# Kernel optimization log

Hardware: AMD Instinct MI355X
Metric: run time of the kernel (lower is better)

The kernel has to match this reference:

```python
import jax, jax.numpy as jnp
import numpy as np

B, L, D, H, FF, V, NL = 1024, 200, 128, 4, 512, 100001, 2
DK = D // H
EPS = 1e-5


def layer_norm(x, w, b):
    mu = jnp.mean(x, axis=-1, keepdims=True)
    var = jnp.mean(jnp.square(x - mu), axis=-1, keepdims=True)
    return (x - mu) * jax.lax.rsqrt(var + EPS) * w + b


def setup_inputs() -> dict:
    key = jax.random.key(0)
    ks = jax.random.split(key, 32)
    s = 0.02
    d = {}
    d["batch_seqs"] = jax.random.randint(ks[0], (B, L), 0, V, dtype=jnp.int32)
    d["token_emb"] = jax.random.normal(ks[1], (V, D), jnp.float32) * s
    d["pos_emb"] = jax.random.normal(ks[2], (L, D), jnp.float32) * s
    # per-layer stacked params, leading axis = layer
    d["Wq"] = jax.random.normal(ks[3], (NL, D, D), jnp.float32) * s
    d["bq"] = jnp.zeros((NL, D), jnp.float32)
    d["Wk"] = jax.random.normal(ks[4], (NL, D, D), jnp.float32) * s
    d["bk"] = jnp.zeros((NL, D), jnp.float32)
    d["Wv"] = jax.random.normal(ks[5], (NL, D, D), jnp.float32) * s
    d["bv"] = jnp.zeros((NL, D), jnp.float32)
    d["Wo"] = jax.random.normal(ks[6], (NL, D, D), jnp.float32) * s
    d["bo"] = jnp.zeros((NL, D), jnp.float32)
    d["ln1_w"] = jnp.ones((NL, D), jnp.float32)
    d["ln1_b"] = jnp.zeros((NL, D), jnp.float32)
    d["ln2_w"] = jnp.ones((NL, D), jnp.float32)
    d["ln2_b"] = jnp.zeros((NL, D), jnp.float32)
    d["W1"] = jax.random.normal(ks[7], (NL, D, FF), jnp.float32) * s
    d["b1"] = jnp.zeros((NL, FF), jnp.float32)
    d["W2"] = jax.random.normal(ks[8], (NL, FF, D), jnp.float32) * s
    d["b2"] = jnp.zeros((NL, D), jnp.float32)
    d["fc_W"] = jax.random.normal(ks[9], (L * D, D), jnp.float32) * s
    d["fc_b"] = jnp.zeros((D,), jnp.float32)
    return d


def reference(batch_seqs, token_emb, pos_emb, Wq, bq, Wk, bk, Wv, bv, Wo, bo,
              ln1_w, ln1_b, ln2_w, ln2_b, W1, b1, W2, b2, fc_W, fc_b):
    # key-padding mask: [B,1,1,L] (broadcasts over heads and queries)
    mask = (batch_seqs > 0)[:, None, None, :]
    x = token_emb[batch_seqs] + pos_emb[None, :, :]  # [B,L,D]
    scale = 1.0 / jnp.sqrt(jnp.float32(DK))
    for i in range(NL):
        h = layer_norm(x, ln1_w[i], ln1_b[i])
        q = (h @ Wq[i] + bq[i]).reshape(B, L, H, DK)
        k = (h @ Wk[i] + bk[i]).reshape(B, L, H, DK)
        v = (h @ Wv[i] + bv[i]).reshape(B, L, H, DK)
        scores = jnp.einsum('bqhd,bkhd->bhqk', q, k) * scale
        scores = jnp.where(mask, scores, -1e9)
        p = jax.nn.softmax(scores, axis=-1)
        attn = jnp.einsum('bhqk,bkhd->bqhd', p, v).reshape(B, L, D)
        x = x + (attn @ Wo[i] + bo[i])
        h = layer_norm(x, ln2_w[i], ln2_b[i])
        ffn = jax.nn.gelu(h @ W1[i] + b1[i], approximate=False) @ W2[i] + b2[i]
        x = x + ffn
    # FlattenLayers: flatten [B, L*D] -> Linear -> [B, D]
    out = x.reshape(B, L * D) @ fc_W + fc_b
    return out
```

## Files before the change

kernel.cpp:

```cpp
#include <hip/hip_runtime.h>
#include <math.h>

typedef unsigned short u16;
typedef unsigned int u32;
typedef __attribute__((ext_vector_type(8))) short bf16x8;
typedef __attribute__((ext_vector_type(4))) float f32x4;

#define Bx 1024
#define Lx 200
#define Dx 128
#define FFx 512
#define Mx (Bx*Lx)
#define PVP 232
#define TSP 40

__device__ __forceinline__ u16 f2bf(float f) {
  u32 u = __float_as_uint(f);
  u32 r = (u + 0x7fffu + ((u >> 16) & 1u)) >> 16;
  return (u16)r;
}

__device__ __forceinline__ float gelu_f(float v) {
  float z = v * fmaf(v * v, 0.0713548163f, 1.5957691216f);
  float e = __expf(-z);
  return v * __builtin_amdgcn_rcpf(1.0f + e);
}

union BFCV { u32 u[4]; bf16x8 h; };

struct CvtJobs {
  const float* src[13];
  u16* dst[13];
  int N[13];
  int ks[13];
  int bstart[14];
};

__global__ void k_cvt_all(CvtJobs J) {
  const int b = blockIdx.x;
  int j = 0;
  #pragma unroll 1
  while (b >= J.bstart[j + 1]) ++j;
  const float* __restrict__ src = J.src[j];
  u16* __restrict__ dst = J.dst[j];
  const int N = J.N[j], k_steps = J.ks[j];
  int id = (b - J.bstart[j]) * 256 + threadIdx.x;
  int lane = id & 63;
  int rest = id >> 6;
  int kst = rest % k_steps;
  int ntile = rest / k_steps;
  int n = ntile * 16 + (lane & 15);
  int kb = kst * 32 + ((lane >> 4) << 3);
  const float* sp = src + (size_t)kb * N + n;
  u32 w[4];
  #pragma unroll
  for (int jj = 0; jj < 4; ++jj) {
    u32 lo = f2bf(sp[(size_t)(2 * jj) * N]);
    u32 hi = f2bf(sp[(size_t)(2 * jj + 1) * N]);
    w[jj] = lo | (hi << 16);
  }
  ((uint4*)dst)[id] = make_uint4(w[0], w[1], w[2], w[3]);
}

__global__ void k_embed(const int* __restrict__ seq, const float* __restrict__ tok,
                        const float* __restrict__ pos, float* __restrict__ x) {
  const int i = blockIdx.x * 256 + threadIdx.x;
  const int row = i >> 5, c = i & 31;
  const int t = seq[row];
  const int l = row % Lx;
  const float4 a = ((const float4*)tok)[(size_t)t * 32 + c];
  const float4 p = ((const float4*)pos)[l * 32 + c];
  ((float4*)x)[i] = make_float4(a.x + p.x, a.y + p.y, a.z + p.z, a.w + p.w);
}

__device__ __forceinline__ void reg_ln(const float* __restrict__ xr,
                                       const float* __restrict__ ln_w,
                                       const float* __restrict__ ln_b,
                                       int quad, bf16x8 af[4]) {
  float v[32];
  float s = 0.f, sq = 0.f;
  #pragma unroll
  for (int kst = 0; kst < 4; ++kst) {
    float4 a = *(const float4*)(xr + kst * 32);
    float4 b = *(const float4*)(xr + kst * 32 + 4);
    v[kst * 8 + 0] = a.x; v[kst * 8 + 1] = a.y; v[kst * 8 + 2] = a.z; v[kst * 8 + 3] = a.w;
    v[kst * 8 + 4] = b.x; v[kst * 8 + 5] = b.y; v[kst * 8 + 6] = b.z; v[kst * 8 + 7] = b.w;
  }
  #pragma unroll
  for (int i = 0; i < 32; ++i) { s += v[i]; sq = fmaf(v[i], v[i], sq); }
  s  += __shfl_xor(s, 16);  s  += __shfl_xor(s, 32);
  sq += __shfl_xor(sq, 16); sq += __shfl_xor(sq, 32);
  float mu = s * 0.0078125f;
  float rr = rsqrtf(fmaf(-mu, mu, sq * 0.0078125f) + 1e-5f);
  #pragma unroll
  for (int kst = 0; kst < 4; ++kst) {
    const float* lwp = ln_w + kst * 32 + quad * 8;
    const float* lbp = ln_b + kst * 32 + quad * 8;
    float4 lw0 = *(const float4*)(lwp);
    float4 lw1 = *(const float4*)(lwp + 4);
    float4 lb0 = *(const float4*)(lbp);
    float4 lb1 = *(const float4*)(lbp + 4);
    float hw[8] = {lw0.x, lw0.y, lw0.z, lw0.w, lw1.x, lw1.y, lw1.z, lw1.w};
    float hb[8] = {lb0.x, lb0.y, lb0.z, lb0.w, lb1.x, lb1.y, lb1.z, lb1.w};
    BFCV cv;
    #pragma unroll
    for (int j = 0; j < 4; ++j) {
      float h0 = fmaf((v[kst * 8 + 2 * j]     - mu) * rr, hw[2 * j],     hb[2 * j]);
      float h1 = fmaf((v[kst * 8 + 2 * j + 1] - mu) * rr, hw[2 * j + 1], hb[2 * j + 1]);
      cv.u[j] = (u32)f2bf(h0) | ((u32)f2bf(h1) << 16);
    }
    af[kst] = cv.h;
  }
}

__global__ __launch_bounds__(256, 4)
void k_qkv(const float* __restrict__ x, const float* __restrict__ ln_w,
           const float* __restrict__ ln_b, const u16* __restrict__ Wqkvs,
           const float* __restrict__ bq, const float* __restrict__ bk,
           const float* __restrict__ bv,
           u16* __restrict__ qo, u16* __restrict__ ko, u16* __restrict__ vo) {
  const int tid = threadIdx.x;
  const int row0 = blockIdx.x * 64;
  const int lane = tid & 63, wv = tid >> 6;
  const int l15 = lane & 15, quad = lane >> 4;
  const int m0 = wv * 16;

  bf16x8 af[4];
  reg_ln(x + (size_t)(row0 + m0 + l15) * Dx + quad * 8, ln_w, ln_b, quad, af);

  int bl[4], ll[4];
  #pragma unroll
  for (int r = 0; r < 4; ++r) {
    int gr = row0 + m0 + quad * 4 + r;
    bl[r] = gr / 200;
    ll[r] = gr - bl[r] * 200;
  }

  const float scale = 0.17677669529663687f;
  #pragma unroll
  for (int nt = 0; nt < 24; ++nt) {
    f32x4 acc = (f32x4){0.f, 0.f, 0.f, 0.f};
    const u16* wb = Wqkvs + ((size_t)(nt * 4) * 64 + lane) * 8;
    #pragma unroll
    for (int kst = 0; kst < 4; ++kst) {
      bf16x8 bfr = *(const bf16x8*)(wb + kst * 64 * 8);
      acc = __builtin_amdgcn_mfma_f32_16x16x32_bf16(af[kst], bfr, acc, 0, 0, 0);
    }
    const int col = (nt & 7) * 16 + l15;
    const int head = col >> 5, dk = col & 31;
    if (nt < 8) {
      float bb = bq[col];
      #pragma unroll
      for (int r = 0; r < 4; ++r)
        qo[((size_t)(bl[r] * 4 + head) * 200 + ll[r]) * 32 + dk] = f2bf((acc[r] + bb) * scale);
    } else if (nt < 16) {
      float bb = bk[col];
      #pragma unroll
      for (int r = 0; r < 4; ++r)
        ko[((size_t)(bl[r] * 4 + head) * 200 + ll[r]) * 32 + dk] = f2bf(acc[r] + bb);
    } else {
      float bb = bv[col];
      #pragma unroll
      for (int r = 0; r < 4; ++r)
        vo[((size_t)(bl[r] * 4 + head) * 200 + ll[r]) * 32 + dk] = f2bf(acc[r] + bb);
    }
  }
}

__global__ __launch_bounds__(256, 3)
void k_attn2(const u16* __restrict__ q, const u16* __restrict__ k,
             const u16* __restrict__ v, const int* __restrict__ seq,
             u16* __restrict__ attn) {
  __shared__ float smask[224];
  __shared__ __align__(16) u16 vt[32 * PVP];
  __shared__ __align__(16) u16 Pb[4][16 * PVP];
  const int tid = threadIdx.x;
  const int bl = blockIdx.x >> 3, head = (blockIdx.x >> 1) & 3;
  const int bh = blockIdx.x >> 1;
  const int half = blockIdx.x & 1;
  const int lane = tid & 63, wv = tid >> 6;
  const int l15 = lane & 15, quad = lane >> 4;

  if (tid < 224)
    smask[tid] = (tid < 200 && seq[bl * 200 + tid] > 0) ? 0.f : -1e9f;
  #pragma unroll 1
  for (int e = tid; e < 800; e += 256) {
    int l = e >> 2, g = (e & 3) * 8;
    uint4 pv = *(const uint4*)(v + ((size_t)bh * 200 + l) * 32 + g);
    const u16* pw = (const u16*)&pv;
    #pragma unroll
    for (int j = 0; j < 8; ++j) vt[(g + j) * PVP + l] = pw[j];
  }
  #pragma unroll 1
  for (int e = tid; e < 1024; e += 256) {
    int rr = e >> 5, cc = 200 + (e & 31);
    vt[rr * PVP + cc] = 0;
  }
  __syncthreads();

  float msk[14];
  #pragma unroll
  for (int nt = 0; nt < 14; ++nt) msk[nt] = smask[nt * 16 + l15];

  const u16* qbase = q + (size_t)bh * 200 * 32;
  const u16* kbase = k + (size_t)bh * 200 * 32;
  u16* Pw = Pb[wv];

  const int mt0 = half ? 7 : 0;
  const int mte = half ? 13 : 7;
  #pragma unroll 1
  for (int mt = mt0 + wv; mt < mte; mt += 4) {
    bf16x8 qf = *(const bf16x8*)(qbase + (mt * 16 + l15) * 32 + quad * 8);
    f32x4 s[14];
    #pragma unroll
    for (int nt = 0; nt < 14; ++nt) {
      bf16x8 kf = *(const bf16x8*)(kbase + (nt * 16 + l15) * 32 + quad * 8);
      s[nt] = __builtin_amdgcn_mfma_f32_16x16x32_bf16(qf, kf, (f32x4){0.f, 0.f, 0.f, 0.f}, 0, 0, 0);
    }
    float rmax[4] = {-1e30f, -1e30f, -1e30f, -1e30f};
    #pragma unroll
    for (int nt = 0; nt < 14; ++nt) {
      #pragma unroll
      for (int r = 0; r < 4; ++r) {
        s[nt][r] += msk[nt];
        rmax[r] = fmaxf(rmax[r], s[nt][r]);
      }
    }
    #pragma unroll
    for (int m = 1; m < 16; m <<= 1) {
      #pragma unroll
      for (int r = 0; r < 4; ++r) rmax[r] = fmaxf(rmax[r], __shfl_xor(rmax[r], m));
    }
    float rsum[4] = {0.f, 0.f, 0.f, 0.f};
    #pragma unroll
    for (int nt = 0; nt < 14; ++nt) {
      #pragma unroll
      for (int r = 0; r < 4; ++r) {
        float p = __expf(s[nt][r] - rmax[r]);
        s[nt][r] = p;
        rsum[r] += p;
      }
    }
    #pragma unroll
    for (int m = 1; m < 16; m <<= 1) {
      #pragma unroll
      for (int r = 0; r < 4; ++r) rsum[r] += __shfl_xor(rsum[r], m);
    }
    float inv[4];
    #pragma unroll
    for (int r = 0; r < 4; ++r) inv[r] = 1.0f / rsum[r];
    #pragma unroll
    for (int nt = 0; nt < 14; ++nt) {
      #pragma unroll
      for (int r = 0; r < 4; ++r)
        Pw[(quad * 4 + r) * PVP + nt * 16 + l15] = f2bf(s[nt][r]);
    }
    __asm__ __volatile__("s_waitcnt lgkmcnt(0)" ::: "memory");
    f32x4 o0 = (f32x4){0.f, 0.f, 0.f, 0.f}, o1 = (f32x4){0.f, 0.f, 0.f, 0.f};
    #pragma unroll
    for (int kst = 0; kst < 7; ++kst) {
      bf16x8 pf  = *(const bf16x8*)&Pw[l15 * PVP + kst * 32 + quad * 8];
      bf16x8 vf0 = *(const bf16x8*)&vt[l15 * PVP + kst * 32 + quad * 8];
      bf16x8 vf1 = *(const bf16x8*)&vt[(16 + l15) * PVP + kst * 32 + quad * 8];
      o0 = __builtin_amdgcn_mfma_f32_16x16x32_bf16(pf, vf0, o0, 0, 0, 0);
      o1 = __builtin_amdgcn_mfma_f32_16x16x32_bf16(pf, vf1, o1, 0, 0, 0);
    }
    #pragma unroll
    for (int r = 0; r < 4; ++r) {
      int row = mt * 16 + quad * 4 + r;
      if (row < 200) {
        u16* op = attn + ((size_t)bl * 200 + row) * 128 + head * 32;
        op[l15]      = f2bf(o0[r] * inv[r]);
        op[16 + l15] = f2bf(o1[r] * inv[r]);
      }
    }
  }
}

__global__ __launch_bounds__(256, 4)
void k_oproj(const u16* __restrict__ a, const u16* __restrict__ Wos,
             const float* __restrict__ bo, float* __restrict__ x) {
  const int tid = threadIdx.x;
  const int lane = tid & 63, wv = tid >> 6;
  const int l15 = lane & 15, quad = lane >> 4;
  const size_t m0 = (size_t)blockIdx.x * 64 + wv * 16;
  f32x4 acc[8];
  #pragma unroll
  for (int i = 0; i < 8; ++i) acc[i] = (f32x4){0.f, 0.f, 0.f, 0.f};
  #pragma unroll
  for (int kst = 0; kst < 4; ++kst) {
    bf16x8 af = *(const bf16x8*)(a + (m0 + l15) * Dx + kst * 32 + quad * 8);
    const u16* wb = Wos + (kst * 64 + lane) * 8;
    #pragma unroll
    for (int nt = 0; nt < 8; ++nt) {
      bf16x8 bf = *(const bf16x8*)(wb + nt * (4 * 64 * 8));
      acc[nt] = __builtin_amdgcn_mfma_f32_16x16x32_bf16(af, bf, acc[nt], 0, 0, 0);
    }
  }
  #pragma unroll
  for (int nt = 0; nt < 8; ++nt) {
    int col = nt * 16 + l15;
    float bb = bo[col];
    #pragma unroll
    for (int r = 0; r < 4; ++r) {
      size_t idx = (m0 + quad * 4 + r) * Dx + col;
      x[idx] += acc[nt][r] + bb;
    }
  }
}

__global__ __launch_bounds__(512, 4)
void k_ffn(float* __restrict__ x, const float* __restrict__ ln_w,
           const float* __restrict__ ln_b,
           const u16* __restrict__ W1s, const float* __restrict__ b1,
           const u16* __restrict__ W2s, const float* __restrict__ b2) {
  __shared__ __align__(16) u16 smem[5120 + 8192 + 8192];
  u16* ts  = smem;
  u16* w1b = smem + 5120;
  u16* w2b = smem + 13312;
  const int tid = threadIdx.x;
  const size_t row0 = (size_t)blockIdx.x * 128;
  const int lane = tid & 63, wv = tid >> 6;
  const int l15 = lane & 15, quad = lane >> 4;
  const int m0 = wv * 16;
  const int snt = wv, soff = lane;

  bf16x8 af[4];
  reg_ln(x + (row0 + m0 + l15) * (size_t)Dx + quad * 8, ln_w, ln_b, quad, af);

  ((uint4*)w1b)[tid] = ((const uint4*)(W1s + (size_t)(snt * 4) * 512))[soff];
  ((uint4*)w2b)[tid] = ((const uint4*)(W2s + (size_t)(snt * 16) * 512))[soff];
  __syncthreads();

  f32x4 acc2[8];
  #pragma unroll
  for (int i = 0; i < 8; ++i) acc2[i] = (f32x4){0.f, 0.f, 0.f, 0.f};

  #pragma unroll 1
  for (int ch = 0; ch < 4; ++ch) {
    f32x4 acc1[8];
    #pragma unroll
    for (int i = 0; i < 8; ++i) acc1[i] = (f32x4){0.f, 0.f, 0.f, 0.f};
    #pragma unroll
    for (int kst = 0; kst < 4; ++kst) {
      uint4 stg;
      if (kst < 3)
        stg = ((const uint4*)(W1s + (size_t)((ch * 8 + snt) * 4 + kst + 1) * 512))[soff];
      const u16* wb = w1b + (kst & 1) * 4096;
      #pragma unroll
      for (int nt = 0; nt < 8; ++nt) {
        bf16x8 bfr = *(const bf16x8*)&wb[nt * 512 + lane * 8];
        acc1[nt] = __builtin_amdgcn_mfma_f32_16x16x32_bf16(af[kst], bfr, acc1[nt], 0, 0, 0);
      }
      if (kst < 3)
        ((uint4*)(w1b + ((kst + 1) & 1) * 4096))[tid] = stg;
      __syncthreads();
    }
    #pragma unroll
    for (int p = 0; p < 4; ++p) {
      uint4 stg2, stg1;
      const bool s2  = (p < 3);
      const bool s1n = (p == 3) && (ch < 3);
      if (s2)
        stg2 = ((const uint4*)(W2s + (size_t)(snt * 16 + ch * 4 + p + 1) * 512))[soff];
      if (s1n) {
        stg1 = ((const uint4*)(W1s + (size_t)((ch + 1) * 8 + snt) * 4 * 512))[soff];
        stg2 = ((const uint4*)(W2s + (size_t)(snt * 16 + (ch + 1) * 4) * 512))[soff];
      }
      #pragma unroll
      for (int q2 = 0; q2 < 2; ++q2) {
        const int ntg = 2 * p + q2;
        float bb = b1[ch * 128 + ntg * 16 + l15];
        #pragma unroll
        for (int r = 0; r < 4; ++r)
          ts[(m0 + quad * 4 + r) * TSP + q2 * 16 + l15] =
              f2bf(gelu_f(acc1[ntg][r] + bb));
      }
      __asm__ __volatile__("s_waitcnt lgkmcnt(0)" ::: "memory");
      bf16x8 tf = *(const bf16x8*)&ts[(m0 + l15) * TSP + quad * 8];
      const u16* wb = w2b + (p & 1) * 4096;
      #pragma unroll
      for (int nt = 0; nt < 8; ++nt) {
        bf16x8 bfr = *(const bf16x8*)&wb[nt * 512 + lane * 8];
        acc2[nt] = __builtin_amdgcn_mfma_f32_16x16x32_bf16(tf, bfr, acc2[nt], 0, 0, 0);
      }
      if (s2)
        ((uint4*)(w2b + ((p + 1) & 1) * 4096))[tid] = stg2;
      if (s1n) {
        ((uint4*)w1b)[tid] = stg1;
        ((uint4*)w2b)[tid] = stg2;
      }
      __syncthreads();
    }
  }
  #pragma unroll
  for (int nt = 0; nt < 8; ++nt) {
    int col = nt * 16 + l15;
    float bb = b2[col];
    #pragma unroll
    for (int r = 0; r < 4; ++r) {
      size_t idx = (row0 + m0 + quad * 4 + r) * Dx + col;
      x[idx] += acc2[nt][r] + bb;
    }
  }
}

__global__ __launch_bounds__(256, 4)
void k_fc(const float* __restrict__ x, const u16* __restrict__ fcWs,
          float* __restrict__ part) {
  const int tid = threadIdx.x;
  const int lane = tid & 63, wv = tid >> 6;
  const int l15 = lane & 15, quad = lane >> 4;
  const int m0 = blockIdx.x * 64 + wv * 16;
  const int ky = blockIdx.y;
  f32x4 acc[8];
  #pragma unroll
  for (int i = 0; i < 8; ++i) acc[i] = (f32x4){0.f, 0.f, 0.f, 0.f};
  const float* xp = x + (size_t)(m0 + l15) * 25600 + quad * 8;
  #pragma unroll 1
  for (int kst = ky * 25; kst < ky * 25 + 25; ++kst) {
    float4 xa = *(const float4*)(xp + kst * 32);
    float4 xb2 = *(const float4*)(xp + kst * 32 + 4);
    bf16x8 af;
    af[0] = (short)f2bf(xa.x);  af[1] = (short)f2bf(xa.y);
    af[2] = (short)f2bf(xa.z);  af[3] = (short)f2bf(xa.w);
    af[4] = (short)f2bf(xb2.x); af[5] = (short)f2bf(xb2.y);
    af[6] = (short)f2bf(xb2.z); af[7] = (short)f2bf(xb2.w);
    const u16* wb = fcWs + ((size_t)kst * 64 + lane) * 8;
    #pragma unroll
    for (int nt = 0; nt < 8; ++nt) {
      bf16x8 bf = *(const bf16x8*)(wb + (size_t)nt * (800 * 64 * 8));
      acc[nt] = __builtin_amdgcn_mfma_f32_16x16x32_bf16(af, bf, acc[nt], 0, 0, 0);
    }
  }
  float* pp = part + (size_t)ky * (Bx * Dx);
  #pragma unroll
  for (int nt = 0; nt < 8; ++nt) {
    #pragma unroll
    for (int r = 0; r < 4; ++r) {
      pp[(size_t)(m0 + quad * 4 + r) * Dx + nt * 16 + l15] = acc[nt][r];
    }
  }
}

__global__ void k_fcred(const float* __restrict__ part, const float* __restrict__ fcb,
                        float* __restrict__ out) {
  int i = blockIdx.x * 256 + threadIdx.x;
  float s = fcb[i & 127];
  #pragma unroll
  for (int k = 0; k < 32; ++k) s += part[(size_t)k * (Bx * Dx) + i];
  out[i] = s;
}

extern "C" void kernel_launch(void* const* d_in, const int* in_sizes, int n_in,
                              void* d_out, int out_size, void* d_ws, size_t ws_size,
                              hipStream_t stream) {
  const int*   seq  = (const int*)d_in[0];
  const float* tok  = (const float*)d_in[1];
  const float* pos  = (const float*)d_in[2];
  const float* Wq   = (const float*)d_in[3];
  const float* bq   = (const float*)d_in[4];
  const float* Wk   = (const float*)d_in[5];
  const float* bk   = (const float*)d_in[6];
  const float* Wv   = (const float*)d_in[7];
  const float* bv   = (const float*)d_in[8];
  const float* Wo   = (const float*)d_in[9];
  const float* bo   = (const float*)d_in[10];
  const float* ln1w = (const float*)d_in[11];
  const float* ln1b = (const float*)d_in[12];
  const float* ln2w = (const float*)d_in[13];
  const float* ln2b = (const float*)d_in[14];
  const float* W1   = (const float*)d_in[15];
  const float* b1   = (const float*)d_in[16];
  const float* W2   = (const float*)d_in[17];
  const float* b2   = (const float*)d_in[18];
  const float* fcW  = (const float*)d_in[19];
  const float* fcb  = (const float*)d_in[20];
  float* out = (float*)d_out;

  char* ws = (char*)d_ws;
  const size_t XB = (size_t)Mx * Dx * 4;
  const size_t WBSZ = 7340032;

  int nc = 4;
  for (int t = 1; t <= 4; t <<= 1) {
    size_t qsz = (size_t)(Bx / t) * 51200;
    if (XB + 4 * qsz + WBSZ <= ws_size) { nc = t; break; }
  }
  const int BC = Bx / nc;
  const size_t qsz = (size_t)BC * 51200;

  float* x    = (float*)ws;
  u16* qb     = (u16*)(ws + XB);
  u16* kb     = (u16*)(ws + XB + qsz);
  u16* vb     = (u16*)(ws + XB + 2 * qsz);
  u16* ab     = (u16*)(ws + XB + 3 * qsz);
  float* part = (float*)(ws + XB);
  char* WB    = ws + XB + 4 * qsz;
  u16* W1s0   = (u16*)(WB);
  u16* W1s1   = (u16*)(WB + 131072);
  u16* W2s0   = (u16*)(WB + 262144);
  u16* W2s1   = (u16*)(WB + 393216);
  u16* Wos0   = (u16*)(WB + 524288);
  u16* Wos1   = (u16*)(WB + 557056);
  u16* Wqkvs0 = (u16*)(WB + 589824);
  u16* Wqkvs1 = (u16*)(WB + 688128);
  u16* fcWs   = (u16*)(WB + 786432);

  CvtJobs J;
  const float* srcs[13] = {W1, W1 + Dx * FFx, W2, W2 + FFx * Dx,
                           Wo, Wo + Dx * Dx,
                           Wq, Wk, Wv,
                           Wq + Dx * Dx, Wk + Dx * Dx, Wv + Dx * Dx,
                           fcW};
  u16* dsts[13] = {W1s0, W1s1, W2s0, W2s1, Wos0, Wos1,
                   Wqkvs0, Wqkvs0 + 16384, Wqkvs0 + 32768,
                   Wqkvs1, Wqkvs1 + 16384, Wqkvs1 + 32768,
                   fcWs};
  const int Ns[13]  = {FFx, FFx, Dx, Dx, Dx, Dx, Dx, Dx, Dx, Dx, Dx, Dx, Dx};
  const int kss[13] = {4, 4, 16, 16, 4, 4, 4, 4, 4, 4, 4, 4, 800};
  const int nblk[13] = {32, 32, 32, 32, 8, 8, 8, 8, 8, 8, 8, 8, 1600};
  int acc = 0;
  for (int j = 0; j < 13; ++j) {
    J.src[j] = srcs[j]; J.dst[j] = dsts[j]; J.N[j] = Ns[j]; J.ks[j] = kss[j];
    J.bstart[j] = acc; acc += nblk[j];
  }
  J.bstart[13] = acc;
  k_cvt_all<<<acc, 256, 0, stream>>>(J);

  k_embed<<<25600, 256, 0, stream>>>(seq, tok, pos, x);
  const int cblk = BC * 200 / 64;
  for (int i = 0; i < 2; ++i) {
    const u16* Wqkvs = (i == 0) ? Wqkvs0 : Wqkvs1;
    const u16* Wos   = (i == 0) ? Wos0 : Wos1;
    for (int c = 0; c < nc; ++c) {
      float* xc = x + (size_t)c * BC * 200 * 128;
      const int* seqc = seq + (size_t)c * BC * 200;
      k_qkv<<<cblk, 256, 0, stream>>>(xc, ln1w + i * Dx, ln1b + i * Dx, Wqkvs,
                                      bq + i * Dx, bk + i * Dx, bv + i * Dx,
                                      qb, kb, vb);
      k_attn2<<<BC * 8, 256, 0, stream>>>(qb, kb, vb, seqc, ab);
      k_oproj<<<cblk, 256, 0, stream>>>(ab, Wos, bo + i * Dx, xc);
    }
    k_ffn<<<1600, 512, 0, stream>>>(x, ln2w + i * Dx, ln2b + i * Dx,
                                    (i == 0) ? W1s0 : W1s1, b1 + i * FFx,
                                    (i == 0) ? W2s0 : W2s1, b2 + i * Dx);
  }
  k_fc<<<dim3(16, 32), 256, 0, stream>>>(x, fcWs, part);
  k_fcred<<<512, 256, 0, stream>>>(part, fcb, out);
}
```

Before: 988.9 us.

## Merge attention query halves per block and halve FFN block size

The attention kernel now handles all 13 query tiles of one (batch, head) in a single block instead of splitting them across two blocks. This avoids loading and transposing V and building the mask twice per head, at the cost of half as many blocks. The FFN kernel moves from 512-thread blocks over 128 rows to 256-thread blocks over 64 rows. Each thread now stages two weight vectors per step, which shrinks the transpose scratch buffer and doubles the grid, but each block reloads the full weights for fewer rows.

```diff
diff --git a/kernel.cpp b/kernel.cpp
--- a/kernel.cpp
+++ b/kernel.cpp
@@ -175,9 +175,8 @@
   __shared__ __align__(16) u16 vt[32 * PVP];
   __shared__ __align__(16) u16 Pb[4][16 * PVP];
   const int tid = threadIdx.x;
-  const int bl = blockIdx.x >> 3, head = (blockIdx.x >> 1) & 3;
-  const int bh = blockIdx.x >> 1;
-  const int half = blockIdx.x & 1;
+  const int bl = blockIdx.x >> 2, head = blockIdx.x & 3;
+  const int bh = blockIdx.x;
   const int lane = tid & 63, wv = tid >> 6;
   const int l15 = lane & 15, quad = lane >> 4;
 
@@ -206,10 +205,8 @@
   const u16* kbase = k + (size_t)bh * 200 * 32;
   u16* Pw = Pb[wv];
 
-  const int mt0 = half ? 7 : 0;
-  const int mte = half ? 13 : 7;
   #pragma unroll 1
-  for (int mt = mt0 + wv; mt < mte; mt += 4) {
+  for (int mt = wv; mt < 13; mt += 4) {
     bf16x8 qf = *(const bf16x8*)(qbase + (mt * 16 + l15) * 32 + quad * 8);
     f32x4 s[14];
     #pragma unroll
@@ -309,27 +306,29 @@
   }
 }
 
-__global__ __launch_bounds__(512, 4)
+__global__ __launch_bounds__(256, 4)
 void k_ffn(float* __restrict__ x, const float* __restrict__ ln_w,
            const float* __restrict__ ln_b,
            const u16* __restrict__ W1s, const float* __restrict__ b1,
            const u16* __restrict__ W2s, const float* __restrict__ b2) {
-  __shared__ __align__(16) u16 smem[5120 + 8192 + 8192];
+  __shared__ __align__(16) u16 smem[2560 + 8192 + 8192];
   u16* ts  = smem;
-  u16* w1b = smem + 5120;
-  u16* w2b = smem + 13312;
+  u16* w1b = smem + 2560;
+  u16* w2b = smem + 10752;
   const int tid = threadIdx.x;
-  const size_t row0 = (size_t)blockIdx.x * 128;
+  const size_t row0 = (size_t)blockIdx.x * 64;
   const int lane = tid & 63, wv = tid >> 6;
   const int l15 = lane & 15, quad = lane >> 4;
   const int m0 = wv * 16;
-  const int snt = wv, soff = lane;
+  const int nt0 = tid >> 6, off = tid & 63;
 
   bf16x8 af[4];
   reg_ln(x + (row0 + m0 + l15) * (size_t)Dx + quad * 8, ln_w, ln_b, quad, af);
 
-  ((uint4*)w1b)[tid] = ((const uint4*)(W1s + (size_t)(snt * 4) * 512))[soff];
-  ((uint4*)w2b)[tid] = ((const uint4*)(W2s + (size_t)(snt * 16) * 512))[soff];
+  ((uint4*)w1b)[tid]       = ((const uint4*)(W1s + (size_t)(nt0 * 4) * 512))[off];
+  ((uint4*)w1b)[tid + 256] = ((const uint4*)(W1s + (size_t)((nt0 + 4) * 4) * 512))[off];
+  ((uint4*)w2b)[tid]       = ((const uint4*)(W2s + (size_t)(nt0 * 16) * 512))[off];
+  ((uint4*)w2b)[tid + 256] = ((const uint4*)(W2s + (size_t)((nt0 + 4) * 16) * 512))[off];
   __syncthreads();
 
   f32x4 acc2[8];
@@ -343,29 +342,37 @@
     for (int i = 0; i < 8; ++i) acc1[i] = (f32x4){0.f, 0.f, 0.f, 0.f};
     #pragma unroll
     for (int kst = 0; kst < 4; ++kst) {
-      uint4 stg;
-      if (kst < 3)
-        stg = ((const uint4*)(W1s + (size_t)((ch * 8 + snt) * 4 + kst + 1) * 512))[soff];
+      uint4 s0, s1;
+      if (kst < 3) {
+        s0 = ((const uint4*)(W1s + (size_t)((ch * 8 + nt0) * 4 + kst + 1) * 512))[off];
+        s1 = ((const uint4*)(W1s + (size_t)((ch * 8 + nt0 + 4) * 4 + kst + 1) * 512))[off];
+      }
       const u16* wb = w1b + (kst & 1) * 4096;
       #pragma unroll
       for (int nt = 0; nt < 8; ++nt) {
         bf16x8 bfr = *(const bf16x8*)&wb[nt * 512 + lane * 8];
         acc1[nt] = __builtin_amdgcn_mfma_f32_16x16x32_bf16(af[kst], bfr, acc1[nt], 0, 0, 0);
       }
-      if (kst < 3)
-        ((uint4*)(w1b + ((kst + 1) & 1) * 4096))[tid] = stg;
+      if (kst < 3) {
+        uint4* d = (uint4*)(w1b + ((kst + 1) & 1) * 4096);
+        d[tid] = s0; d[tid + 256] = s1;
+      }
       __syncthreads();
     }
     #pragma unroll
     for (int p = 0; p < 4; ++p) {
-      uint4 stg2, stg1;
+      uint4 s0, s1, t0, t1;
       const bool s2  = (p < 3);
       const bool s1n = (p == 3) && (ch < 3);
-      if (s2)
-        stg2 = ((const uint4*)(W2s + (size_t)(snt * 16 + ch * 4 + p + 1) * 512))[soff];
+      if (s2) {
+        s0 = ((const uint4*)(W2s + (size_t)(nt0 * 16 + ch * 4 + p + 1) * 512))[off];
+        s1 = ((const uint4*)(W2s + (size_t)((nt0 + 4) * 16 + ch * 4 + p + 1) * 512))[off];
+      }
       if (s1n) {
-        stg1 = ((const uint4*)(W1s + (size_t)((ch + 1) * 8 + snt) * 4 * 512))[soff];
-        stg2 = ((const uint4*)(W2s + (size_t)(snt * 16 + (ch + 1) * 4) * 512))[soff];
+        s0 = ((const uint4*)(W1s + (size_t)(((ch + 1) * 8 + nt0) * 4) * 512))[off];
+        s1 = ((const uint4*)(W1s + (size_t)(((ch + 1) * 8 + nt0 + 4) * 4) * 512))[off];
+        t0 = ((const uint4*)(W2s + (size_t)(nt0 * 16 + (ch + 1) * 4) * 512))[off];
+        t1 = ((const uint4*)(W2s + (size_t)((nt0 + 4) * 16 + (ch + 1) * 4) * 512))[off];
       }
       #pragma unroll
       for (int q2 = 0; q2 < 2; ++q2) {
@@ -384,11 +391,13 @@
         bf16x8 bfr = *(const bf16x8*)&wb[nt * 512 + lane * 8];
         acc2[nt] = __builtin_amdgcn_mfma_f32_16x16x32_bf16(tf, bfr, acc2[nt], 0, 0, 0);
       }
-      if (s2)
-        ((uint4*)(w2b + ((p + 1) & 1) * 4096))[tid] = stg2;
+      if (s2) {
+        uint4* d = (uint4*)(w2b + ((p + 1) & 1) * 4096);
+        d[tid] = s0; d[tid + 256] = s1;
+      }
       if (s1n) {
-        ((uint4*)w1b)[tid] = stg1;
-        ((uint4*)w2b)[tid] = stg2;
+        ((uint4*)w1b)[tid] = s0; ((uint4*)w1b)[tid + 256] = s1;
+        ((uint4*)w2b)[tid] = t0; ((uint4*)w2b)[tid + 256] = t1;
       }
       __syncthreads();
     }
@@ -539,10 +548,10 @@
       k_qkv<<<cblk, 256, 0, stream>>>(xc, ln1w + i * Dx, ln1b + i * Dx, Wqkvs,
                                       bq + i * Dx, bk + i * Dx, bv + i * Dx,
                                       qb, kb, vb);
-      k_attn2<<<BC * 8, 256, 0, stream>>>(qb, kb, vb, seqc, ab);
+      k_attn2<<<BC * 4, 256, 0, stream>>>(qb, kb, vb, seqc, ab);
       k_oproj<<<cblk, 256, 0, stream>>>(ab, Wos, bo + i * Dx, xc);
     }
-    k_ffn<<<1600, 512, 0, stream>>>(x, ln2w + i * Dx, ln2b + i * Dx,
+    k_ffn<<<3200, 256, 0, stream>>>(x, ln2w + i * Dx, ln2b + i * Dx,
                                     (i == 0) ? W1s0 : W1s1, b1 + i * FFx,
                                     (i == 0) ? W2s0 : W2s1, b2 + i * Dx);
   }
```

Result: faster. 919.0 us (median of 2 runs) (-7.1%).
